# Kernel optimization log

Hardware: AMD Instinct MI355X
Metric: run time of the kernel (lower is better)

## Reference

```python
import jax, jax.numpy as jnp
import numpy as np
import math

D_MODEL = 256
N_HEADS = 8
HEAD_DIM = D_MODEL // N_HEADS  # 32
N_LEVELS = 4
N_POINTS = 4
SHAPES = [(112, 112), (56, 56), (28, 28), (14, 14)]
LEN_IN = sum(h * w for h, w in SHAPES)  # 16660
BATCH = 1
LEN_Q = LEN_IN


def _grid_init_bias():
    # Faithful to MSDeformAttn._reset_parameters: directional grid init for sampling_offsets bias.
    thetas = np.arange(N_HEADS, dtype=np.float32) * (2.0 * math.pi / N_HEADS)
    grid = np.stack([np.cos(thetas), np.sin(thetas)], -1)
    grid = grid / np.abs(grid).max(-1, keepdims=True)
    grid = np.tile(grid[:, None, None, :], (1, N_LEVELS, N_POINTS, 1)).copy()
    for i in range(N_POINTS):
        grid[:, :, i, :] *= i + 1
    return jnp.asarray(grid.reshape(-1), dtype=jnp.float32)


def setup_inputs() -> dict:
    key = jax.random.key(0)
    ks = jax.random.split(key, 10)
    s = 1.0 / math.sqrt(D_MODEL)
    return {
        "query": jax.random.normal(ks[0], (BATCH, LEN_Q, D_MODEL), jnp.float32),
        "reference_points": jax.random.uniform(ks[1], (BATCH, LEN_Q, N_LEVELS, 2), jnp.float32),
        "input_flatten": jax.random.normal(ks[2], (BATCH, LEN_IN, D_MODEL), jnp.float32),
        "spatial_shapes": jnp.asarray(SHAPES, dtype=jnp.int32),
        "level_start_index": jnp.asarray(np.cumsum([0] + [h * w for h, w in SHAPES])[:-1], dtype=jnp.int32),
        "W_q": jax.random.normal(ks[3], (D_MODEL, D_MODEL), jnp.float32) * s,
        "b_q": jnp.zeros((D_MODEL,), jnp.float32),
        "W_k": jax.random.normal(ks[4], (D_MODEL, D_MODEL), jnp.float32) * s,
        "b_k": jnp.zeros((D_MODEL,), jnp.float32),
        "W_v": jax.random.normal(ks[5], (D_MODEL, D_MODEL), jnp.float32) * s,
        "b_v": jnp.zeros((D_MODEL,), jnp.float32),
        "W_o": jax.random.normal(ks[6], (D_MODEL, D_MODEL), jnp.float32) * s,
        "b_o": jnp.zeros((D_MODEL,), jnp.float32),
        "W_off": jax.random.normal(ks[7], (D_MODEL, N_HEADS * N_LEVELS * N_POINTS * 2), jnp.float32) * 0.01,
        "b_off": _grid_init_bias(),
    }


def _bilinear_sample(img, grid, H, W):
    # img: (B, H*W, D) flattened feature map; grid: (B, Q, P, 2) in [-1, 1] (x, y order).
    # Matches F.grid_sample(mode='bilinear', padding_mode='zeros', align_corners=False).
    B, Q, P, _ = grid.shape
    x = ((grid[..., 0] + 1.0) * W - 1.0) * 0.5
    y = ((grid[..., 1] + 1.0) * H - 1.0) * 0.5
    x0 = jnp.floor(x)
    y0 = jnp.floor(y)
    lx = x - x0
    ly = y - y0
    x0i = x0.astype(jnp.int32)
    y0i = y0.astype(jnp.int32)

    def gather(yi, xi, w):
        valid = (xi >= 0) & (xi < W) & (yi >= 0) & (yi < H)
        idx = jnp.clip(yi, 0, H - 1) * W + jnp.clip(xi, 0, W - 1)
        v = jnp.take_along_axis(img, idx.reshape(B, Q * P, 1), axis=1)
        return v.reshape(B, Q, P, -1) * (w * valid)[..., None]

    return (gather(y0i, x0i, (1.0 - ly) * (1.0 - lx))
            + gather(y0i, x0i + 1, (1.0 - ly) * lx)
            + gather(y0i + 1, x0i, ly * (1.0 - lx))
            + gather(y0i + 1, x0i + 1, ly * lx))


def reference(query, reference_points, input_flatten, spatial_shapes, level_start_index,
              W_q, b_q, W_k, b_k, W_v, b_v, W_o, b_o, W_off, b_off):
    N, Lq, C = query.shape
    M, D, L, P = N_HEADS, HEAD_DIM, N_LEVELS, N_POINTS

    q = query @ W_q + b_q                                   # (N, Lq, C)
    value = (input_flatten @ W_v + b_v).reshape(N, -1, M, D)
    key_h = (input_flatten @ W_k + b_k).reshape(N, -1, M, D)

    offsets = (q @ W_off + b_off).reshape(N, Lq, M, L, P, 2)
    # offset_normalizer = (W_l, H_l) per level
    norm = jnp.stack([spatial_shapes[:, 1], spatial_shapes[:, 0]], -1).astype(q.dtype)
    loc = reference_points[:, :, None, :, None, :] + offsets / norm[None, None, None, :, None, :]
    grids = 2.0 * loc - 1.0                                  # (N, Lq, M, L, P, 2)

    samp_v, samp_k = [], []
    start = 0
    for lid, (H, W) in enumerate(SHAPES):
        end = start + H * W
        v_l = value[:, start:end].transpose(0, 2, 1, 3).reshape(N * M, H * W, D)
        k_l = key_h[:, start:end].transpose(0, 2, 1, 3).reshape(N * M, H * W, D)
        g_l = grids[:, :, :, lid].transpose(0, 2, 1, 3, 4).reshape(N * M, Lq, P, 2)
        samp_v.append(_bilinear_sample(v_l, g_l, H, W))      # (N*M, Lq, P, D)
        samp_k.append(_bilinear_sample(k_l, g_l, H, W))
        start = end

    v_s = jnp.stack(samp_v, axis=2).reshape(N, M, Lq, L, P, D)
    k_s = jnp.stack(samp_k, axis=2).reshape(N, M, Lq, L, P, D)

    qh = q.reshape(N, Lq, M, D)
    logits = jnp.einsum('nqmd,nmqlpd->nmqlp', qh, k_s) / math.sqrt(D)
    attn = jax.nn.softmax(logits.reshape(N, M, Lq, L * P), axis=-1).reshape(N, M, Lq, L, P)

    out = jnp.einsum('nmqlp,nmqlpd->nqmd', attn, v_s).reshape(N, Lq, C)
    return out @ W_o + b_o
```

## Files before the change

### kernel.cpp

```cpp
#include <hip/hip_runtime.h>
#include <hip/hip_bf16.h>
#include <math.h>

#define LEN_IN   16660
#define D_MODEL  256
#define N_HEADS  8

typedef __attribute__((ext_vector_type(8))) short short8v;
typedef __attribute__((ext_vector_type(4))) float f32x4;
typedef _Float16 f16x2 __attribute__((ext_vector_type(2)));
typedef _Float16 f16x8 __attribute__((ext_vector_type(8)));

__device__ __forceinline__ unsigned short f2h(float f) {
  union { unsigned short u; _Float16 h; } c;
  c.h = (_Float16)f;
  return c.u;
}
__device__ __forceinline__ float h2f(unsigned short u) {
  union { unsigned short u; _Float16 h; } c;
  c.u = u;
  return (float)c.h;
}
__device__ __forceinline__ f16x2 u2h(unsigned u) {
  union { unsigned u; f16x2 h; } c;
  c.u = u;
  return c.h;
}

__global__ __launch_bounds__(256) void prep_B(
    const float* __restrict__ Wq, const float* __restrict__ Wk,
    const float* __restrict__ Wv, const float* __restrict__ Woff,
    const float* __restrict__ Wo,
    const float* __restrict__ bq, const float* __restrict__ boff,
    unsigned short* __restrict__ Btq, unsigned short* __restrict__ Btk,
    unsigned short* __restrict__ Btv, unsigned short* __restrict__ Btoff,
    unsigned short* __restrict__ Bto, float* __restrict__ bqo) {
  int b = blockIdx.x;
  int tid = threadIdx.x;
  if (b == 80) {
    float s = boff[tid];
    for (int i = 0; i < 256; i++) s += bq[i] * Woff[(size_t)i * 256 + tid];
    bqo[tid] = s;
    return;
  }
  __shared__ float tile[64][65];
  int mat = b >> 4, t = b & 15;
  int ti = t >> 2, tj = t & 3;
  const float* W = (mat == 0) ? Wq : (mat == 1) ? Wk : (mat == 2) ? Wv
                 : (mat == 3) ? Woff : Wo;
  unsigned short* Bt = (mat == 0) ? Btq : (mat == 1) ? Btk : (mat == 2) ? Btv
                     : (mat == 3) ? Btoff : Bto;
  #pragma unroll
  for (int i = 0; i < 16; i++) {
    int idx = tid + i * 256;
    int kr = idx >> 6, nc = idx & 63;
    tile[kr][nc] = W[(size_t)(ti * 64 + kr) * 256 + tj * 64 + nc];
  }
  __syncthreads();
  #pragma unroll
  for (int i = 0; i < 16; i++) {
    int idx = tid + i * 256;
    int nr = idx >> 6, kc = idx & 63;
    Bt[(size_t)(tj * 64 + nr) * 256 + ti * 64 + kc] = f2h(tile[kc][nr]);
  }
}

__global__ __launch_bounds__(256) void gemm_wqo(
    const float* __restrict__ Wq, const unsigned short* __restrict__ Btoff,
    unsigned short* __restrict__ Btqo) {
  const int P = 40;
  __shared__ short As[64 * P], Bs[64 * P];
  int tid = threadIdx.x;
  int m0 = blockIdx.x * 64, n0 = blockIdx.y * 64;
  int w = tid >> 6, l = tid & 63;
  int r = l & 15, g = l >> 4;
  int mi = (w >> 1) * 32, ni = (w & 1) * 32;
  int sm = tid >> 2, sp = tid & 3;

  f32x4 acc[2][2];
  #pragma unroll
  for (int a = 0; a < 2; a++)
    #pragma unroll
    for (int b = 0; b < 2; b++) acc[a][b] = (f32x4){0.f, 0.f, 0.f, 0.f};

  for (int k0 = 0; k0 < 256; k0 += 32) {
    const float* src = Wq + (size_t)(m0 + sm) * 256 + k0 + sp * 8;
    float4 u0 = *(const float4*)src;
    float4 u1 = *(const float4*)(src + 4);
    f16x8 hv = {(_Float16)u0.x, (_Float16)u0.y, (_Float16)u0.z, (_Float16)u0.w,
                (_Float16)u1.x, (_Float16)u1.y, (_Float16)u1.z, (_Float16)u1.w};
    *(f16x8*)&As[sm * P + sp * 8] = hv;
    *(short8v*)&Bs[sm * P + sp * 8] =
        *(const short8v*)&Btoff[(size_t)(n0 + sm) * 256 + k0 + sp * 8];
    __syncthreads();
    f16x8 af[2], bf[2];
    #pragma unroll
    for (int a = 0; a < 2; a++)
      af[a] = *(f16x8*)&As[(mi + a * 16 + r) * P + g * 8];
    #pragma unroll
    for (int b = 0; b < 2; b++)
      bf[b] = *(f16x8*)&Bs[(ni + b * 16 + r) * P + g * 8];
    #pragma unroll
    for (int a = 0; a < 2; a++)
      #pragma unroll
      for (int b = 0; b < 2; b++)
        acc[a][b] = __builtin_amdgcn_mfma_f32_16x16x32_f16(af[a], bf[b], acc[a][b], 0, 0, 0);
    __syncthreads();
  }
  #pragma unroll
  for (int a = 0; a < 2; a++)
    #pragma unroll
    for (int b = 0; b < 2; b++) {
      int col = n0 + ni + b * 16 + r;
      #pragma unroll
      for (int i = 0; i < 4; i++) {
        int row = m0 + mi + a * 16 + g * 4 + i;
        Btqo[(size_t)col * 256 + row] = f2h(acc[a][b][i]);
      }
    }
}

__global__ __launch_bounds__(256) void gemm_qkv(
    const float* __restrict__ query, const float* __restrict__ inp,
    const unsigned short* __restrict__ Btq,
    const unsigned short* __restrict__ Btk,
    const unsigned short* __restrict__ Btv,
    const unsigned short* __restrict__ Btqo,
    const float* __restrict__ bq, const float* __restrict__ bk,
    const float* __restrict__ bv, const float* __restrict__ bqo,
    unsigned short* __restrict__ qp_out, unsigned* __restrict__ kv_out,
    unsigned short* __restrict__ offs_out, int M) {
  const int P = 72;
  __shared__ short As[64 * P], B1[64 * P], B2[64 * P];
  int z = blockIdx.z;
  const float* A = (z == 1) ? inp : query;
  const unsigned short* Bt1 = (z == 0) ? Btq : (z == 1) ? Btk : Btqo;
  int tid = threadIdx.x;
  int m0 = blockIdx.x * 64, n0 = blockIdx.y * 64;
  int w = tid >> 6, l = tid & 63;
  int r = l & 15, g = l >> 4;
  int mi = (w >> 1) * 32, ni = (w & 1) * 32;
  int srow = tid >> 2, sch = (tid & 3) * 16;

  f32x4 acc1[2][2], acc2[2][2];
  #pragma unroll
  for (int a = 0; a < 2; a++)
    #pragma unroll
    for (int b = 0; b < 2; b++) {
      acc1[a][b] = (f32x4){0.f, 0.f, 0.f, 0.f};
      acc2[a][b] = (f32x4){0.f, 0.f, 0.f, 0.f};
    }

  for (int k0 = 0; k0 < 256; k0 += 64) {
    int gm = m0 + srow;
    f16x8 h0, h1;
    if (gm < M) {
      const float* src = A + (size_t)gm * 256 + k0 + sch;
      float4 u0 = *(const float4*)src;
      float4 u1 = *(const float4*)(src + 4);
      float4 u2 = *(const float4*)(src + 8);
      float4 u3 = *(const float4*)(src + 12);
      h0 = (f16x8){(_Float16)u0.x, (_Float16)u0.y, (_Float16)u0.z, (_Float16)u0.w,
                   (_Float16)u1.x, (_Float16)u1.y, (_Float16)u1.z, (_Float16)u1.w};
      h1 = (f16x8){(_Float16)u2.x, (_Float16)u2.y, (_Float16)u2.z, (_Float16)u2.w,
                   (_Float16)u3.x, (_Float16)u3.y, (_Float16)u3.z, (_Float16)u3.w};
    } else {
      h0 = (f16x8){0, 0, 0, 0, 0, 0, 0, 0};
      h1 = h0;
    }
    *(f16x8*)&As[srow * P + sch] = h0;
    *(f16x8*)&As[srow * P + sch + 8] = h1;
    {
      const unsigned short* bsrc = Bt1 + (size_t)(n0 + srow) * 256 + k0 + sch;
      *(short8v*)&B1[srow * P + sch] = *(const short8v*)bsrc;
      *(short8v*)&B1[srow * P + sch + 8] = *(const short8v*)(bsrc + 8);
    }
    if (z == 1) {
      const unsigned short* bsrc = Btv + (size_t)(n0 + srow) * 256 + k0 + sch;
      *(short8v*)&B2[srow * P + sch] = *(const short8v*)bsrc;
      *(short8v*)&B2[srow * P + sch + 8] = *(const short8v*)(bsrc + 8);
    }
    __syncthreads();

    f16x8 af[2][2], b1f[2][2], b2f[2][2];
    #pragma unroll
    for (int a = 0; a < 2; a++)
      #pragma unroll
      for (int ks = 0; ks < 2; ks++)
        af[a][ks] = *(f16x8*)&As[(mi + a * 16 + r) * P + ks * 32 + g * 8];
    #pragma unroll
    for (int b = 0; b < 2; b++)
      #pragma unroll
      for (int ks = 0; ks < 2; ks++)
        b1f[b][ks] = *(f16x8*)&B1[(ni + b * 16 + r) * P + ks * 32 + g * 8];
    if (z == 1) {
      #pragma unroll
      for (int b = 0; b < 2; b++)
        #pragma unroll
        for (int ks = 0; ks < 2; ks++)
          b2f[b][ks] = *(f16x8*)&B2[(ni + b * 16 + r) * P + ks * 32 + g * 8];
    }
    #pragma unroll
    for (int a = 0; a < 2; a++)
      #pragma unroll
      for (int b = 0; b < 2; b++)
        #pragma unroll
        for (int ks = 0; ks < 2; ks++) {
          acc1[a][b] = __builtin_amdgcn_mfma_f32_16x16x32_f16(af[a][ks], b1f[b][ks], acc1[a][b], 0, 0, 0);
          if (z == 1)
            acc2[a][b] = __builtin_amdgcn_mfma_f32_16x16x32_f16(af[a][ks], b2f[b][ks], acc2[a][b], 0, 0, 0);
        }
    __syncthreads();
  }

  #pragma unroll
  for (int a = 0; a < 2; a++)
    #pragma unroll
    for (int b = 0; b < 2; b++) {
      int col = n0 + ni + b * 16 + r;
      if (z == 0) {
        float bc = bq[col];
        #pragma unroll
        for (int i = 0; i < 4; i++) {
          int row = m0 + mi + a * 16 + g * 4 + i;
          if (row < M) qp_out[(size_t)row * 256 + col] = f2h(acc1[a][b][i] + bc);
        }
      } else if (z == 1) {
        float bkc = bk[col], bvc = bv[col];
        int hh = col >> 5, cc = col & 31;
        #pragma unroll
        for (int i = 0; i < 4; i++) {
          int row = m0 + mi + a * 16 + g * 4 + i;
          if (row < M) {
            unsigned kh = f2h(acc1[a][b][i] + bkc);
            unsigned vh = f2h(acc2[a][b][i] + bvc);
            kv_out[((size_t)hh * LEN_IN + row) * 32 + cc] = kh | (vh << 16);
          }
        }
      } else {
        float bc = bqo[col];
        #pragma unroll
        for (int i = 0; i < 4; i++) {
          int row = m0 + mi + a * 16 + g * 4 + i;
          if (row < M) offs_out[(size_t)row * 256 + col] = f2h(acc1[a][b][i] + bc);
        }
      }
    }
}

__global__ __launch_bounds__(256) void gemm_out(
    const unsigned short* __restrict__ A,
    const unsigned short* __restrict__ Bt,
    const float* __restrict__ bias, float* __restrict__ C, int M) {
  const int P = 72;
  __shared__ short As[64 * P], Bs[64 * P];
  int tid = threadIdx.x;
  int m0 = blockIdx.x * 64, n0 = blockIdx.y * 64;
  int w = tid >> 6, l = tid & 63;
  int r = l & 15, g = l >> 4;
  int mi = (w >> 1) * 32, ni = (w & 1) * 32;
  int srow = tid >> 2, sch = (tid & 3) * 16;

  f32x4 acc[2][2];
  #pragma unroll
  for (int a = 0; a < 2; a++)
    #pragma unroll
    for (int b = 0; b < 2; b++) acc[a][b] = (f32x4){0.f, 0.f, 0.f, 0.f};

  for (int k0 = 0; k0 < 256; k0 += 64) {
    int gm = m0 + srow;
    short8v a0 = {0, 0, 0, 0, 0, 0, 0, 0}, a1 = a0;
    if (gm < M) {
      const unsigned short* src = A + (size_t)gm * 256 + k0 + sch;
      a0 = *(const short8v*)src;
      a1 = *(const short8v*)(src + 8);
    }
    *(short8v*)&As[srow * P + sch] = a0;
    *(short8v*)&As[srow * P + sch + 8] = a1;
    const unsigned short* bsrc = Bt + (size_t)(n0 + srow) * 256 + k0 + sch;
    *(short8v*)&Bs[srow * P + sch] = *(const short8v*)bsrc;
    *(short8v*)&Bs[srow * P + sch + 8] = *(const short8v*)(bsrc + 8);
    __syncthreads();

    f16x8 af[2][2], bf[2][2];
    #pragma unroll
    for (int a = 0; a < 2; a++)
      #pragma unroll
      for (int ks = 0; ks < 2; ks++)
        af[a][ks] = *(f16x8*)&As[(mi + a * 16 + r) * P + ks * 32 + g * 8];
    #pragma unroll
    for (int b = 0; b < 2; b++)
      #pragma unroll
      for (int ks = 0; ks < 2; ks++)
        bf[b][ks] = *(f16x8*)&Bs[(ni + b * 16 + r) * P + ks * 32 + g * 8];
    #pragma unroll
    for (int a = 0; a < 2; a++)
      #pragma unroll
      for (int b = 0; b < 2; b++)
        #pragma unroll
        for (int ks = 0; ks < 2; ks++)
          acc[a][b] = __builtin_amdgcn_mfma_f32_16x16x32_f16(af[a][ks], bf[b][ks], acc[a][b], 0, 0, 0);
    __syncthreads();
  }
  #pragma unroll
  for (int a = 0; a < 2; a++)
    #pragma unroll
    for (int b = 0; b < 2; b++) {
      int col = n0 + ni + b * 16 + r;
      float bc = bias[col];
      #pragma unroll
      for (int i = 0; i < 4; i++) {
        int row = m0 + mi + a * 16 + g * 4 + i;
        if (row < M) C[(size_t)row * 256 + col] = acc[a][b][i] + bc;
      }
    }
}

__global__ __launch_bounds__(256) void sample_attn(
    const unsigned short* __restrict__ qp,
    const unsigned short* __restrict__ offs,
    const float* __restrict__ rp,
    const unsigned* __restrict__ kv,
    unsigned short* __restrict__ attn_out) {
  __shared__ float lbuf[4][16];
  __shared__ float ebuf[4][16];
  __shared__ float vbuf[4][16][36];

  int tid = threadIdx.x;
  int wslot = tid >> 6;
  int lane = tid & 63;
  int wid = blockIdx.x * 4 + wslot;
  int q = wid >> 3;
  int h = wid & 7;

  int pt = lane >> 2;
  int c8 = (lane & 3) * 8;
  int l5 = lane & 31;

  float offv = h2f(offs[(size_t)q * 256 + h * 32 + l5]);
  float rpv = (l5 < 8) ? rp[(size_t)q * 8 + l5] : 0.f;

  int l = pt >> 2, pp = pt & 3;
  int W = 112 >> l;
  int start = (int)((50176u - (50176u >> (2 * l))) / 3u);

  float off_x = __shfl(offv, l * 8 + pp * 2 + 0, 32);
  float off_y = __shfl(offv, l * 8 + pp * 2 + 1, 32);
  float rp_x = __shfl(rpv, l * 2 + 0, 32);
  float rp_y = __shfl(rpv, l * 2 + 1, 32);

  float x = rp_x * (float)W + off_x - 0.5f;
  float y = rp_y * (float)W + off_y - 0.5f;
  float x0f = floorf(x), y0f = floorf(y);
  float lx = x - x0f, ly = y - y0f;
  int x0 = (int)x0f, y0 = (int)y0f;
  float wx0 = 1.f - lx, wy0 = 1.f - ly;
  float tw[4] = {wy0 * wx0, wy0 * lx, ly * wx0, ly * lx};

  const unsigned* kvh = kv + (size_t)h * LEN_IN * 32 + c8;

  f16x2 acc[8];
  #pragma unroll
  for (int j = 0; j < 8; j++) acc[j] = (f16x2){(_Float16)0.f, (_Float16)0.f};

  #pragma unroll
  for (int tap = 0; tap < 4; tap++) {
    int yy = y0 + (tap >> 1), xx = x0 + (tap & 1);
    bool valid = ((unsigned)xx < (unsigned)W) & ((unsigned)yy < (unsigned)W);
    float wgt = valid ? tw[tap] : 0.f;
    int pix = valid ? (start + yy * W + xx) : start;
    const unsigned* p = kvh + (size_t)pix * 32;
    uint4 u0 = *(const uint4*)p;
    uint4 u1 = *(const uint4*)(p + 4);
    _Float16 wh = (_Float16)wgt;
    f16x2 w2 = {wh, wh};
    acc[0] += w2 * u2h(u0.x);
    acc[1] += w2 * u2h(u0.y);
    acc[2] += w2 * u2h(u0.z);
    acc[3] += w2 * u2h(u0.w);
    acc[4] += w2 * u2h(u1.x);
    acc[5] += w2 * u2h(u1.y);
    acc[6] += w2 * u2h(u1.z);
    acc[7] += w2 * u2h(u1.w);
  }

  uint4 qa = *(const uint4*)(qp + (size_t)q * 256 + h * 32 + c8);
  float dot = 0.f;
  f16x2 kp;
  kp[0] = acc[0][0]; kp[1] = acc[1][0];
  dot = __builtin_amdgcn_fdot2(u2h(qa.x), kp, dot, false);
  kp[0] = acc[2][0]; kp[1] = acc[3][0];
  dot = __builtin_amdgcn_fdot2(u2h(qa.y), kp, dot, false);
  kp[0] = acc[4][0]; kp[1] = acc[5][0];
  dot = __builtin_amdgcn_fdot2(u2h(qa.z), kp, dot, false);
  kp[0] = acc[6][0]; kp[1] = acc[7][0];
  dot = __builtin_amdgcn_fdot2(u2h(qa.w), kp, dot, false);
  dot += __shfl_xor(dot, 1, 64);
  dot += __shfl_xor(dot, 2, 64);
  if ((lane & 3) == 0) lbuf[wslot][pt] = dot * 0.17677669529663687f;

  float4 v0 = {(float)acc[0][1], (float)acc[1][1], (float)acc[2][1], (float)acc[3][1]};
  float4 v1 = {(float)acc[4][1], (float)acc[5][1], (float)acc[6][1], (float)acc[7][1]};
  *(float4*)&vbuf[wslot][pt][c8] = v0;
  *(float4*)&vbuf[wslot][pt][c8 + 4] = v1;
  __syncthreads();

  float lg = lbuf[wslot][lane & 15];
  float m = lg;
  m = fmaxf(m, __shfl_xor(m, 1, 64));
  m = fmaxf(m, __shfl_xor(m, 2, 64));
  m = fmaxf(m, __shfl_xor(m, 4, 64));
  m = fmaxf(m, __shfl_xor(m, 8, 64));
  float e = __expf(lg - m);
  float s = e;
  s += __shfl_xor(s, 1, 64);
  s += __shfl_xor(s, 2, 64);
  s += __shfl_xor(s, 4, 64);
  s += __shfl_xor(s, 8, 64);
  if (lane < 16) ebuf[wslot][lane] = e;
  float inv = 1.f / s;
  __syncthreads();

  if (lane < 32) {
    float o = 0.f;
    #pragma unroll
    for (int p = 0; p < 16; p++) o += ebuf[wslot][p] * vbuf[wslot][p][lane];
    attn_out[(size_t)q * 256 + h * 32 + lane] = f2h(o * inv);
  }
}

extern "C" void kernel_launch(void* const* d_in, const int* in_sizes, int n_in,
                              void* d_out, int out_size, void* d_ws, size_t ws_size,
                              hipStream_t stream) {
  const float* query = (const float*)d_in[0];
  const float* rp    = (const float*)d_in[1];
  const float* inp   = (const float*)d_in[2];
  const float* W_q   = (const float*)d_in[5];
  const float* b_q   = (const float*)d_in[6];
  const float* W_k   = (const float*)d_in[7];
  const float* b_k   = (const float*)d_in[8];
  const float* W_v   = (const float*)d_in[9];
  const float* b_v   = (const float*)d_in[10];
  const float* W_o   = (const float*)d_in[11];
  const float* b_o   = (const float*)d_in[12];
  const float* W_off = (const float*)d_in[13];
  const float* b_off = (const float*)d_in[14];
  float* out = (float*)d_out;

  const size_t nelem = (size_t)LEN_IN * D_MODEL;
  unsigned short* qp    = (unsigned short*)d_ws;
  unsigned short* offsb = qp + nelem;
  unsigned short* attn  = offsb + nelem;
  unsigned* kvp = (unsigned*)(attn + nelem);
  unsigned short* Btq   = (unsigned short*)(kvp + nelem);
  unsigned short* Btk   = Btq + 256 * 256;
  unsigned short* Btv   = Btk + 256 * 256;
  unsigned short* Btoff = Btv + 256 * 256;
  unsigned short* Bto   = Btoff + 256 * 256;
  unsigned short* Btqo  = Bto + 256 * 256;
  float* bqo = (float*)(Btqo + 256 * 256);

  dim3 blk(256);
  dim3 ggrid((LEN_IN + 63) / 64, D_MODEL / 64);
  dim3 ggrid3((LEN_IN + 63) / 64, D_MODEL / 64, 3);

  prep_B<<<81, blk, 0, stream>>>(W_q, W_k, W_v, W_off, W_o, b_q, b_off,
                                 Btq, Btk, Btv, Btoff, Bto, bqo);
  gemm_wqo<<<dim3(4, 4), blk, 0, stream>>>(W_q, Btoff, Btqo);

  gemm_qkv<<<ggrid3, blk, 0, stream>>>(query, inp, Btq, Btk, Btv, Btqo,
                                       b_q, b_k, b_v, bqo,
                                       qp, kvp, offsb, LEN_IN);

  int n_blocks = LEN_IN * N_HEADS / 4;
  sample_attn<<<n_blocks, blk, 0, stream>>>(qp, offsb, rp, kvp, attn);

  gemm_out<<<ggrid, blk, 0, stream>>>(attn, Bto, b_o, out, LEN_IN);
}
```

Measured before the change: 130.2 us.

## Pre-convert activations to fp16 and enlarge GEMM M-tile to 128

Adds a kernel that converts query and input_flatten to fp16 once, so the QKV GEMM reads half-width activations instead of converting fp32 in each block. Before, the query was re-read and re-converted by both the z=0 and z=2 slices. Both the QKV and output GEMMs now use 128x64 tiles, with each wave computing 64x32, to raise MFMA work per loaded B tile. The trade-offs are an extra launch with a full fp32 read and fp16 write pass, more registers and shared memory per block, and fewer blocks.

```diff
diff --git a/kernel.cpp b/kernel.cpp
--- a/kernel.cpp
+++ b/kernel.cpp
@@ -25,6 +25,22 @@
   union { unsigned u; f16x2 h; } c;
   c.u = u;
   return c.h;
+}
+
+__global__ __launch_bounds__(256) void cvt16(
+    const float* __restrict__ a, const float* __restrict__ b,
+    unsigned short* __restrict__ a16, unsigned short* __restrict__ b16) {
+  const int nq = (LEN_IN * D_MODEL) / 4;
+  int i = blockIdx.x * 256 + threadIdx.x;
+  int stride = gridDim.x * 256;
+  for (int qd = i; qd < nq; qd += stride) {
+    float4 va = ((const float4*)a)[qd];
+    ushort4 ha = {f2h(va.x), f2h(va.y), f2h(va.z), f2h(va.w)};
+    ((ushort4*)a16)[qd] = ha;
+    float4 vb = ((const float4*)b)[qd];
+    ushort4 hb = {f2h(vb.x), f2h(vb.y), f2h(vb.z), f2h(vb.w)};
+    ((ushort4*)b16)[qd] = hb;
+  }
 }
 
 __global__ __launch_bounds__(256) void prep_B(
@@ -121,7 +137,7 @@
 }
 
 __global__ __launch_bounds__(256) void gemm_qkv(
-    const float* __restrict__ query, const float* __restrict__ inp,
+    const unsigned short* __restrict__ q16, const unsigned short* __restrict__ in16,
     const unsigned short* __restrict__ Btq,
     const unsigned short* __restrict__ Btk,
     const unsigned short* __restrict__ Btv,
@@ -131,20 +147,21 @@
     unsigned short* __restrict__ qp_out, unsigned* __restrict__ kv_out,
     unsigned short* __restrict__ offs_out, int M) {
   const int P = 72;
-  __shared__ short As[64 * P], B1[64 * P], B2[64 * P];
+  __shared__ short As[128 * P], B1[64 * P], B2[64 * P];
   int z = blockIdx.z;
-  const float* A = (z == 1) ? inp : query;
+  const unsigned short* A = (z == 1) ? in16 : q16;
   const unsigned short* Bt1 = (z == 0) ? Btq : (z == 1) ? Btk : Btqo;
   int tid = threadIdx.x;
-  int m0 = blockIdx.x * 64, n0 = blockIdx.y * 64;
+  int m0 = blockIdx.x * 128, n0 = blockIdx.y * 64;
   int w = tid >> 6, l = tid & 63;
   int r = l & 15, g = l >> 4;
-  int mi = (w >> 1) * 32, ni = (w & 1) * 32;
-  int srow = tid >> 2, sch = (tid & 3) * 16;
-
-  f32x4 acc1[2][2], acc2[2][2];
-  #pragma unroll
-  for (int a = 0; a < 2; a++)
+  int mi = (w >> 1) * 64, ni = (w & 1) * 32;
+  int arow = tid >> 1, ach = (tid & 1) * 32;
+  int brow = tid >> 2, bch = (tid & 3) * 16;
+
+  f32x4 acc1[4][2], acc2[4][2];
+  #pragma unroll
+  for (int a = 0; a < 4; a++)
     #pragma unroll
     for (int b = 0; b < 2; b++) {
       acc1[a][b] = (f32x4){0.f, 0.f, 0.f, 0.f};
@@ -152,39 +169,34 @@
     }
 
   for (int k0 = 0; k0 < 256; k0 += 64) {
-    int gm = m0 + srow;
-    f16x8 h0, h1;
+    int gm = m0 + arow;
+    short8v a0 = {0,0,0,0,0,0,0,0}, a1 = a0, a2 = a0, a3 = a0;
     if (gm < M) {
-      const float* src = A + (size_t)gm * 256 + k0 + sch;
-      float4 u0 = *(const float4*)src;
-      float4 u1 = *(const float4*)(src + 4);
-      float4 u2 = *(const float4*)(src + 8);
-      float4 u3 = *(const float4*)(src + 12);
-      h0 = (f16x8){(_Float16)u0.x, (_Float16)u0.y, (_Float16)u0.z, (_Float16)u0.w,
-                   (_Float16)u1.x, (_Float16)u1.y, (_Float16)u1.z, (_Float16)u1.w};
-      h1 = (f16x8){(_Float16)u2.x, (_Float16)u2.y, (_Float16)u2.z, (_Float16)u2.w,
-                   (_Float16)u3.x, (_Float16)u3.y, (_Float16)u3.z, (_Float16)u3.w};
-    } else {
-      h0 = (f16x8){0, 0, 0, 0, 0, 0, 0, 0};
-      h1 = h0;
-    }
-    *(f16x8*)&As[srow * P + sch] = h0;
-    *(f16x8*)&As[srow * P + sch + 8] = h1;
+      const unsigned short* src = A + (size_t)gm * 256 + k0 + ach;
+      a0 = *(const short8v*)src;
+      a1 = *(const short8v*)(src + 8);
+      a2 = *(const short8v*)(src + 16);
+      a3 = *(const short8v*)(src + 24);
+    }
+    *(short8v*)&As[arow * P + ach] = a0;
+    *(short8v*)&As[arow * P + ach + 8] = a1;
+    *(short8v*)&As[arow * P + ach + 16] = a2;
+    *(short8v*)&As[arow * P + ach + 24] = a3;
     {
-      const unsigned short* bsrc = Bt1 + (size_t)(n0 + srow) * 256 + k0 + sch;
-      *(short8v*)&B1[srow * P + sch] = *(const short8v*)bsrc;
-      *(short8v*)&B1[srow * P + sch + 8] = *(const short8v*)(bsrc + 8);
+      const unsigned short* bsrc = Bt1 + (size_t)(n0 + brow) * 256 + k0 + bch;
+      *(short8v*)&B1[brow * P + bch] = *(const short8v*)bsrc;
+      *(short8v*)&B1[brow * P + bch + 8] = *(const short8v*)(bsrc + 8);
     }
     if (z == 1) {
-      const unsigned short* bsrc = Btv + (size_t)(n0 + srow) * 256 + k0 + sch;
-      *(short8v*)&B2[srow * P + sch] = *(const short8v*)bsrc;
-      *(short8v*)&B2[srow * P + sch + 8] = *(const short8v*)(bsrc + 8);
-    }
-    __syncthreads();
-
-    f16x8 af[2][2], b1f[2][2], b2f[2][2];
-    #pragma unroll
-    for (int a = 0; a < 2; a++)
+      const unsigned short* bsrc = Btv + (size_t)(n0 + brow) * 256 + k0 + bch;
+      *(short8v*)&B2[brow * P + bch] = *(const short8v*)bsrc;
+      *(short8v*)&B2[brow * P + bch + 8] = *(const short8v*)(bsrc + 8);
+    }
+    __syncthreads();
+
+    f16x8 af[4][2], b1f[2][2], b2f[2][2];
+    #pragma unroll
+    for (int a = 0; a < 4; a++)
       #pragma unroll
       for (int ks = 0; ks < 2; ks++)
         af[a][ks] = *(f16x8*)&As[(mi + a * 16 + r) * P + ks * 32 + g * 8];
@@ -201,7 +213,7 @@
           b2f[b][ks] = *(f16x8*)&B2[(ni + b * 16 + r) * P + ks * 32 + g * 8];
     }
     #pragma unroll
-    for (int a = 0; a < 2; a++)
+    for (int a = 0; a < 4; a++)
       #pragma unroll
       for (int b = 0; b < 2; b++)
         #pragma unroll
@@ -214,7 +226,7 @@
   }
 
   #pragma unroll
-  for (int a = 0; a < 2; a++)
+  for (int a = 0; a < 4; a++)
     #pragma unroll
     for (int b = 0; b < 2; b++) {
       int col = n0 + ni + b * 16 + r;
@@ -253,38 +265,43 @@
     const unsigned short* __restrict__ Bt,
     const float* __restrict__ bias, float* __restrict__ C, int M) {
   const int P = 72;
-  __shared__ short As[64 * P], Bs[64 * P];
+  __shared__ short As[128 * P], Bs[64 * P];
   int tid = threadIdx.x;
-  int m0 = blockIdx.x * 64, n0 = blockIdx.y * 64;
+  int m0 = blockIdx.x * 128, n0 = blockIdx.y * 64;
   int w = tid >> 6, l = tid & 63;
   int r = l & 15, g = l >> 4;
-  int mi = (w >> 1) * 32, ni = (w & 1) * 32;
-  int srow = tid >> 2, sch = (tid & 3) * 16;
-
-  f32x4 acc[2][2];
-  #pragma unroll
-  for (int a = 0; a < 2; a++)
+  int mi = (w >> 1) * 64, ni = (w & 1) * 32;
+  int arow = tid >> 1, ach = (tid & 1) * 32;
+  int brow = tid >> 2, bch = (tid & 3) * 16;
+
+  f32x4 acc[4][2];
+  #pragma unroll
+  for (int a = 0; a < 4; a++)
     #pragma unroll
     for (int b = 0; b < 2; b++) acc[a][b] = (f32x4){0.f, 0.f, 0.f, 0.f};
 
   for (int k0 = 0; k0 < 256; k0 += 64) {
-    int gm = m0 + srow;
-    short8v a0 = {0, 0, 0, 0, 0, 0, 0, 0}, a1 = a0;
+    int gm = m0 + arow;
+    short8v a0 = {0,0,0,0,0,0,0,0}, a1 = a0, a2 = a0, a3 = a0;
     if (gm < M) {
-      const unsigned short* src = A + (size_t)gm * 256 + k0 + sch;
+      const unsigned short* src = A + (size_t)gm * 256 + k0 + ach;
       a0 = *(const short8v*)src;
       a1 = *(const short8v*)(src + 8);
-    }
-    *(short8v*)&As[srow * P + sch] = a0;
-    *(short8v*)&As[srow * P + sch + 8] = a1;
-    const unsigned short* bsrc = Bt + (size_t)(n0 + srow) * 256 + k0 + sch;
-    *(short8v*)&Bs[srow * P + sch] = *(const short8v*)bsrc;
-    *(short8v*)&Bs[srow * P + sch + 8] = *(const short8v*)(bsrc + 8);
-    __syncthreads();
-
-    f16x8 af[2][2], bf[2][2];
-    #pragma unroll
-    for (int a = 0; a < 2; a++)
+      a2 = *(const short8v*)(src + 16);
+      a3 = *(const short8v*)(src + 24);
+    }
+    *(short8v*)&As[arow * P + ach] = a0;
+    *(short8v*)&As[arow * P + ach + 8] = a1;
+    *(short8v*)&As[arow * P + ach + 16] = a2;
+    *(short8v*)&As[arow * P + ach + 24] = a3;
+    const unsigned short* bsrc = Bt + (size_t)(n0 + brow) * 256 + k0 + bch;
+    *(short8v*)&Bs[brow * P + bch] = *(const short8v*)bsrc;
+    *(short8v*)&Bs[brow * P + bch + 8] = *(const short8v*)(bsrc + 8);
+    __syncthreads();
+
+    f16x8 af[4][2], bf[2][2];
+    #pragma unroll
+    for (int a = 0; a < 4; a++)
       #pragma unroll
       for (int ks = 0; ks < 2; ks++)
         af[a][ks] = *(f16x8*)&As[(mi + a * 16 + r) * P + ks * 32 + g * 8];
@@ -294,7 +311,7 @@
       for (int ks = 0; ks < 2; ks++)
         bf[b][ks] = *(f16x8*)&Bs[(ni + b * 16 + r) * P + ks * 32 + g * 8];
     #pragma unroll
-    for (int a = 0; a < 2; a++)
+    for (int a = 0; a < 4; a++)
       #pragma unroll
       for (int b = 0; b < 2; b++)
         #pragma unroll
@@ -303,7 +320,7 @@
     __syncthreads();
   }
   #pragma unroll
-  for (int a = 0; a < 2; a++)
+  for (int a = 0; a < 4; a++)
     #pragma unroll
     for (int b = 0; b < 2; b++) {
       int col = n0 + ni + b * 16 + r;
@@ -448,7 +465,9 @@
   float* out = (float*)d_out;
 
   const size_t nelem = (size_t)LEN_IN * D_MODEL;
-  unsigned short* qp    = (unsigned short*)d_ws;
+  unsigned short* q16   = (unsigned short*)d_ws;
+  unsigned short* in16  = q16 + nelem;
+  unsigned short* qp    = in16 + nelem;
   unsigned short* offsb = qp + nelem;
   unsigned short* attn  = offsb + nelem;
   unsigned* kvp = (unsigned*)(attn + nelem);
@@ -461,14 +480,15 @@
   float* bqo = (float*)(Btqo + 256 * 256);
 
   dim3 blk(256);
-  dim3 ggrid((LEN_IN + 63) / 64, D_MODEL / 64);
-  dim3 ggrid3((LEN_IN + 63) / 64, D_MODEL / 64, 3);
-
+  dim3 ggrid((LEN_IN + 127) / 128, D_MODEL / 64);
+  dim3 ggrid3((LEN_IN + 127) / 128, D_MODEL / 64, 3);
+
+  cvt16<<<2048, blk, 0, stream>>>(query, inp, q16, in16);
   prep_B<<<81, blk, 0, stream>>>(W_q, W_k, W_v, W_off, W_o, b_q, b_off,
                                  Btq, Btk, Btv, Btoff, Bto, bqo);
   gemm_wqo<<<dim3(4, 4), blk, 0, stream>>>(W_q, Btoff, Btqo);
 
-  gemm_qkv<<<ggrid3, blk, 0, stream>>>(query, inp, Btq, Btk, Btv, Btqo,
+  gemm_qkv<<<ggrid3, blk, 0, stream>>>(q16, in16, Btq, Btk, Btv, Btqo,
                                        b_q, b_k, b_v, bqo,
                                        qp, kvp, offsb, LEN_IN);
 
```

Result: no change. 131.3 us (+0.8%).
